# Kernel optimization log

Hardware: AMD Instinct MI355X
Metric: run time of the kernel (lower is better)

Reference implementation:

```python
import jax, jax.numpy as jnp
import numpy as np

B, CIN, COUT, K, H, W_SP = 16, 16, 16, 3, 384, 384


def setup_inputs() -> dict:
    key = jax.random.key(0)
    k1, k2 = jax.random.split(key)
    x = jax.random.normal(k1, (B, CIN, H, W_SP), dtype=jnp.float32)
    W = jax.random.normal(k2, (COUT, CIN, K, K), dtype=jnp.float32) * 0.05
    return {"x": x, "W": W}


def reference(x, W):
    b, cin, h, w = x.shape
    cout, _, kh, kw = W.shape
    # torch.where(x < 0, 0, 1): binary activity mask (x == 0 maps to 1)
    mask = (x >= 0).astype(x.dtype)
    # adaptive_avg_pool2d(mask, kh): h % kh == 0 and w % kw == 0, so bins are
    # exact equal-size means -> reshape + mean.  (b, cin, kh, kw)
    att = mask.reshape(b, cin, kh, h // kh, kw, w // kw).mean(axis=(3, 5))
    att = att.reshape(b, cin, kh * kw)
    att = kh * kw * jax.nn.softmax(att, axis=2) - 1.0
    att = 1.0 + jax.nn.sigmoid(att).reshape(b, cin, kh, kw)
    # per-sample modulated weights: (b, cout, cin, kh, kw); broadcast over cout
    wmod = W[None, :, :, :, :] * att[:, None, :, :, :]

    def conv_one(xi, wi):
        # xi: (cin, h, w), wi: (cout, cin, kh, kw); stride 1, padding 1 (same)
        return jax.lax.conv_general_dilated(
            xi[None], wi, window_strides=(1, 1), padding=[(1, 1), (1, 1)],
            dimension_numbers=("NCHW", "OIHW", "NCHW"))[0]

    # equivalent to the groups=b grouped-conv trick, but without materializing
    # the (1, b*cin, h, w) view
    y = jax.vmap(conv_one)(x, wmod)  # (b, cout, h, w)
    return y
```

## Files before the change

kernel.cpp:

```cpp
#include <hip/hip_runtime.h>
#include <hip/hip_bf16.h>
#include <math.h>

#define BB   16
#define CI   16
#define CO   16
#define HH   384
#define WW   384
#define HW   (HH * WW)

#define PW 386

#define TSW 32
#define TSH 16
#define HSW 34
#define HSH 18
#define NPX (HSW * HSH)

typedef __bf16 bfx8 __attribute__((ext_vector_type(8)));
typedef float  f32x4 __attribute__((ext_vector_type(4)));

__device__ __forceinline__ uint32_t pack_bf16(float a, float b) {
  uint32_t ua = __builtin_bit_cast(uint32_t, a);
  uint32_t ub = __builtin_bit_cast(uint32_t, b);
  ua = (ua + 0x7FFFu + ((ua >> 16) & 1u)) >> 16;
  ub = (ub + 0x7FFFu + ((ub >> 16) & 1u)) >> 16;
  return ua | (ub << 16);
}

__device__ __forceinline__ void gl_lds16(const void* g, void* l) {
  __builtin_amdgcn_global_load_lds(
      (const __attribute__((address_space(1))) uint32_t*)g,
      (__attribute__((address_space(3))) uint32_t*)l, 16, 0, 0);
}


__global__ __launch_bounds__(384, 2) void prep_kernel(
    const float* __restrict__ x, uint4* __restrict__ XP,
    int* __restrict__ pooled) {
  const int b   = blockIdx.y;
  const int blk = blockIdx.x;
  const int tid = threadIdx.x;

  const int r  = tid / 96;
  const int c4 = tid - r * 96;
  const int h  = blk * 4 + r;
  const int w  = c4 * 4;
  const float* px = x + ((size_t)b * CI) * HW + (size_t)h * WW + w;

  f32x4 v[CI];
#pragma unroll
  for (int ci = 0; ci < CI; ++ci)
    v[ci] = *(const f32x4*)(px + (size_t)ci * HW);
  __builtin_amdgcn_sched_barrier(0);

  uint4* dst = XP + (((size_t)b * PW + (h + 1)) * PW + (w + 1)) * 2;
#pragma unroll
  for (int p = 0; p < 4; ++p) {
    uint32_t pk[8];
#pragma unroll
    for (int i = 0; i < 8; ++i)
      pk[i] = pack_bf16(v[2 * i][p], v[2 * i + 1][p]);
    uint4 lo, hi;
    lo.x = pk[0]; lo.y = pk[1]; lo.z = pk[2]; lo.w = pk[3];
    hi.x = pk[4]; hi.y = pk[5]; hi.z = pk[6]; hi.w = pk[7];
    dst[2 * p]     = lo;
    dst[2 * p + 1] = hi;
  }

  int cnt[CI];
#pragma unroll
  for (int ci = 0; ci < CI; ++ci)
    cnt[ci] = (v[ci][0] >= 0.f) + (v[ci][1] >= 0.f) + (v[ci][2] >= 0.f) +
              (v[ci][3] >= 0.f);

#pragma unroll
  for (int ci = 0; ci < CI; ++ci) {
#pragma unroll
    for (int s = 1; s < 32; s <<= 1)
      cnt[ci] += __shfl_xor(cnt[ci], s, 64);
  }

  if ((tid & 31) == 0) {
    const int bin = (h >> 7) * 3 + (w >> 7);
#pragma unroll
    for (int ci = 0; ci < CI; ++ci)
      atomicAdd(&pooled[(b * CI + ci) * 9 + bin], cnt[ci]);
  }
}

__global__ __launch_bounds__(384) void border_kernel(uint4* __restrict__ XP) {
  const int b = blockIdx.x;
  const int tid = threadIdx.x;
  const uint4 z = {0u, 0u, 0u, 0u};
  for (int j = tid; j < 1540; j += 384) {
    int pr, pc;
    if (j < 386)       { pr = 0;            pc = j; }
    else if (j < 772)  { pr = PW - 1;       pc = j - 386; }
    else if (j < 1156) { pr = j - 772 + 1;  pc = 0; }
    else               { pr = j - 1156 + 1; pc = PW - 1; }
    uint4* p = XP + (((size_t)b * PW + pr) * PW + pc) * 2;
    p[0] = z; p[1] = z;
  }
}

__global__ __launch_bounds__(256) void att_finish_int(
    const int* __restrict__ pooled, float* __restrict__ att) {
  const int plane = threadIdx.x;
  float v[9];
#pragma unroll
  for (int k = 0; k < 9; ++k)
    v[k] = (float)pooled[plane * 9 + k] * (1.f / 16384.f);
  float m = v[0];
#pragma unroll
  for (int k = 1; k < 9; ++k) m = fmaxf(m, v[k]);
  float e[9], s = 0.f;
#pragma unroll
  for (int k = 0; k < 9; ++k) { e[k] = expf(v[k] - m); s += e[k]; }
  const float inv = 1.f / s;
#pragma unroll
  for (int k = 0; k < 9; ++k) {
    const float a = 9.f * e[k] * inv - 1.f;
    att[plane * 9 + k] = 1.f + 1.f / (1.f + expf(-a));
  }
}

__global__ __launch_bounds__(256) void conv_fast(
    const char* __restrict__ XPc, const float* __restrict__ Wt,
    const float* __restrict__ att, float* __restrict__ y) {
  const int b   = blockIdx.z;
  const int gx0 = blockIdx.x * TSW;
  const int gy0 = blockIdx.y * TSH;
  const int tid = threadIdx.x;

  __shared__ __align__(16) uint32_t sx[NPX * 8];
  __shared__ __align__(16) uint32_t sw[CO * 80];

  const int lane = tid & 63;
  const int wv   = tid >> 6;

  const char* XPb = XPc + (size_t)b * (PW * PW * 32);
#pragma unroll
  for (int i = wv; i < 20; i += 4) {
    const int chunk = i * 64 + lane;
    const int px  = chunk >> 1;
    const int hf  = chunk & 1;
    const int rr  = px / HSW;
    const int cc  = px - rr * HSW;
    const int swz = (cc >> 2) & 1;
    const char* src =
        XPb + (((size_t)(gy0 + rr) * PW + (gx0 + cc)) << 5) + ((hf ^ swz) << 4);
    if (chunk < 2 * NPX) gl_lds16(src, (char*)sx + i * 1024);
  }

#pragma unroll
  for (int i = 0; i < 5; ++i) {
    const int idx  = tid + 256 * i;
    const int cout = idx / 80;
    const int kp   = idx - cout * 80;
    const int k0 = 2 * kp, k1 = 2 * kp + 1;
    const int p0 = k0 >> 4, ci0 = k0 & 15;
    const int p1 = k1 >> 4, ci1 = k1 & 15;
    float v0 = 0.f, v1 = 0.f;
    if (p0 < 9) v0 = Wt[(cout * CI + ci0) * 9 + p0] * att[(b * CI + ci0) * 9 + p0];
    if (p1 < 9) v1 = Wt[(cout * CI + ci1) * 9 + p1] * att[(b * CI + ci1) * 9 + p1];
    sw[cout * 80 + kp] = pack_bf16(v0, v1);
  }
  __syncthreads();

  const int cpix = lane & 15;
  const int h4   = lane >> 4;
  const int hB   = h4 & 1;
  const int pp   = lane >> 5;

  bfx8 aw[5];
  const char* swb = (const char*)sw;
#pragma unroll
  for (int q = 0; q < 5; ++q)
    aw[q] = *(const bfx8*)(swb + cpix * 320 + q * 64 + h4 * 16);

  int Lq[5];
#pragma unroll
  for (int q = 0; q < 5; ++q) {
    int p = 2 * q + pp;
    if (p > 8) p = 8;
    const int dy = p / 3, dx = p - 3 * dy;
    const int ccl = cpix + dx;
    const int swz = (ccl >> 2) & 1;
    Lq[q] = (dy * HSW + ccl) * 32 + 16 * (hB ^ swz);
  }

  const char* sxb = (const char*)sx;
  float* yb = y + ((size_t)b * CO + h4 * 4) * HW + (size_t)gy0 * WW + gx0 + cpix;

#pragma unroll 2
  for (int ri = 0; ri < 4; ++ri) {
    const int r = wv * 4 + ri;
    const int gbase = (r * HSW) * 32;
    f32x4 a0 = {0.f, 0.f, 0.f, 0.f};
    f32x4 a1 = {0.f, 0.f, 0.f, 0.f};
#pragma unroll
    for (int q = 0; q < 5; ++q) {
      const bfx8 b0 = *(const bfx8*)(sxb + gbase + Lq[q]);
      const bfx8 b1 = *(const bfx8*)(sxb + gbase + 512 + Lq[q]);
      a0 = __builtin_amdgcn_mfma_f32_16x16x32_bf16(aw[q], b0, a0, 0, 0, 0);
      a1 = __builtin_amdgcn_mfma_f32_16x16x32_bf16(aw[q], b1, a1, 0, 0, 0);
    }
    float* yr = yb + (size_t)r * WW;
#pragma unroll
    for (int j = 0; j < 4; ++j) {
      __builtin_nontemporal_store(a0[j], &yr[(size_t)j * HW]);
      __builtin_nontemporal_store(a1[j], &yr[(size_t)j * HW + 16]);
    }
  }
}

__global__ __launch_bounds__(256) void pool_kernel(
    const float* __restrict__ x, float* __restrict__ pooled) {
  const int bx = blockIdx.x;
  const int plane = bx / 9;
  const int bin = bx - plane * 9;
  const int br = (bin / 3) * 128;
  const int bc4 = (bin % 3) * 32;
  const float4* xp = (const float4*)(x + (size_t)plane * HW);
  const int tid = threadIdx.x;
  int cnt = 0;
#pragma unroll
  for (int k = 0; k < 16; ++k) {
    const int idx = tid + k * 256;
    const int r = idx >> 5;
    const int c4 = idx & 31;
    const float4 v = xp[(size_t)(br + r) * (WW / 4) + bc4 + c4];
    cnt += (v.x >= 0.f) + (v.y >= 0.f) + (v.z >= 0.f) + (v.w >= 0.f);
  }
#pragma unroll
  for (int s = 32; s > 0; s >>= 1) cnt += __shfl_down(cnt, s);
  __shared__ int wsum[4];
  const int lane = tid & 63, wid = tid >> 6;
  if (lane == 0) wsum[wid] = cnt;
  __syncthreads();
  if (tid == 0)
    pooled[bx] = (float)(wsum[0] + wsum[1] + wsum[2] + wsum[3]) * (1.f / 16384.f);
}

__global__ __launch_bounds__(256) void att_finish(
    const float* __restrict__ pooled, float* __restrict__ att) {
  const int plane = threadIdx.x;
  float v[9];
#pragma unroll
  for (int k = 0; k < 9; ++k) v[k] = pooled[plane * 9 + k];
  float m = v[0];
#pragma unroll
  for (int k = 1; k < 9; ++k) m = fmaxf(m, v[k]);
  float e[9], s = 0.f;
#pragma unroll
  for (int k = 0; k < 9; ++k) { e[k] = expf(v[k] - m); s += e[k]; }
  const float inv = 1.f / s;
#pragma unroll
  for (int k = 0; k < 9; ++k) {
    const float a = 9.f * e[k] * inv - 1.f;
    att[plane * 9 + k] = 1.f + 1.f / (1.f + expf(-a));
  }
}

__global__ __launch_bounds__(256) void conv_legacy(
    const float* __restrict__ x, const float* __restrict__ Wt,
    const float* __restrict__ att, float* __restrict__ y) {
  const int b   = blockIdx.z;
  const int gx0 = blockIdx.x * TSW;
  const int gy0 = blockIdx.y * TSH;
  const int tid = threadIdx.x;
  __shared__ __align__(16) uint32_t sx[NPX * 8];
  __shared__ __align__(16) uint32_t sw[CO * 80];
  const float* xb = x + (size_t)b * CI * HW;
#pragma unroll
  for (int i = 0; i < 5; ++i) {
    const int idx  = tid + 256 * i;
    const int cout = idx / 80;
    const int kp   = idx - cout * 80;
    const int k0 = 2 * kp, k1 = 2 * kp + 1;
    const int p0 = k0 >> 4, ci0 = k0 & 15;
    const int p1 = k1 >> 4, ci1 = k1 & 15;
    float v0 = 0.f, v1 = 0.f;
    if (p0 < 9) v0 = Wt[(cout * CI + ci0) * 9 + p0] * att[(b * CI + ci0) * 9 + p0];
    if (p1 < 9) v1 = Wt[(cout * CI + ci1) * 9 + p1] * att[(b * CI + ci1) * 9 + p1];
    sw[cout * 80 + kp] = pack_bf16(v0, v1);
  }
#pragma unroll
  for (int it = 0; it < 3; ++it) {
    const int pix = tid + 256 * it;
    if (pix < NPX) {
      const int rr = pix / HSW;
      const int cc = pix - rr * HSW;
      const int gr = gy0 - 1 + rr;
      const int gc = gx0 - 1 + cc;
      uint32_t pk[8];
      if (((unsigned)gr < (unsigned)HH) && ((unsigned)gc < (unsigned)WW)) {
        const float* px = xb + (size_t)gr * WW + gc;
#pragma unroll
        for (int i = 0; i < 8; ++i)
          pk[i] = pack_bf16(px[(size_t)(2 * i) * HW], px[(size_t)(2 * i + 1) * HW]);
      } else {
#pragma unroll
        for (int i = 0; i < 8; ++i) pk[i] = 0u;
      }
      const int s = (cc >> 2) & 1;
      uint32_t* dst = &sx[pix * 8];
      uint4 lo, hi;
      lo.x = pk[0]; lo.y = pk[1]; lo.z = pk[2]; lo.w = pk[3];
      hi.x = pk[4]; hi.y = pk[5]; hi.z = pk[6]; hi.w = pk[7];
      *(uint4*)(dst + 4 * s)       = lo;
      *(uint4*)(dst + 4 * (1 - s)) = hi;
    }
  }
  __syncthreads();
  const int lane = tid & 63;
  const int wv   = tid >> 6;
  const int cpix = lane & 15;
  const int h4   = lane >> 4;
  const int hB   = h4 & 1;
  const int pp   = lane >> 5;
  bfx8 aw[5];
  const char* swb = (const char*)sw;
#pragma unroll
  for (int q = 0; q < 5; ++q)
    aw[q] = *(const bfx8*)(swb + cpix * 320 + q * 64 + h4 * 16);
  int Lq[5];
#pragma unroll
  for (int q = 0; q < 5; ++q) {
    int p = 2 * q + pp;
    if (p > 8) p = 8;
    const int dy = p / 3, dx = p - 3 * dy;
    const int ccl = cpix + dx;
    const int swz = (ccl >> 2) & 1;
    Lq[q] = (dy * HSW + ccl) * 32 + 16 * (hB ^ swz);
  }
  const char* sxb = (const char*)sx;
  float* yb = y + ((size_t)b * CO + h4 * 4) * HW + (size_t)gy0 * WW + gx0 + cpix;
#pragma unroll 2
  for (int ri = 0; ri < 4; ++ri) {
    const int r = wv * 4 + ri;
    const int gbase = (r * HSW) * 32;
    f32x4 a0 = {0.f, 0.f, 0.f, 0.f};
    f32x4 a1 = {0.f, 0.f, 0.f, 0.f};
#pragma unroll
    for (int q = 0; q < 5; ++q) {
      const bfx8 b0 = *(const bfx8*)(sxb + gbase + Lq[q]);
      const bfx8 b1 = *(const bfx8*)(sxb + gbase + 512 + Lq[q]);
      a0 = __builtin_amdgcn_mfma_f32_16x16x32_bf16(aw[q], b0, a0, 0, 0, 0);
      a1 = __builtin_amdgcn_mfma_f32_16x16x32_bf16(aw[q], b1, a1, 0, 0, 0);
    }
    float* yr = yb + (size_t)r * WW;
#pragma unroll
    for (int j = 0; j < 4; ++j) {
      yr[(size_t)j * HW]      = a0[j];
      yr[(size_t)j * HW + 16] = a1[j];
    }
  }
}

extern "C" void kernel_launch(void* const* d_in, const int* in_sizes, int n_in,
                              void* d_out, int out_size, void* d_ws,
                              size_t ws_size, hipStream_t stream) {
  const float* x  = (const float*)d_in[0];
  const float* Wt = (const float*)d_in[1];
  float* y = (float*)d_out;
  char* wsb = (char*)d_ws;

  const size_t need = 65536 + (size_t)BB * PW * PW * 32;
  if (ws_size >= need) {
    int*   pooled = (int*)wsb;
    float* att    = (float*)(wsb + 16384);
    uint4* XP     = (uint4*)(wsb + 65536);
    hipMemsetAsync(pooled, 0, BB * CI * 9 * sizeof(int), stream);
    border_kernel<<<dim3(BB), dim3(384), 0, stream>>>(XP);
    prep_kernel<<<dim3(96, BB), dim3(384), 0, stream>>>(x, XP, pooled);
    att_finish_int<<<dim3(1), dim3(256), 0, stream>>>(pooled, att);
    conv_fast<<<dim3(WW / TSW, HH / TSH, BB), dim3(256), 0, stream>>>(
        (const char*)XP, Wt, att, y);
  } else {
    float* pooled = (float*)wsb;
    float* att    = (float*)wsb + 4096;
    pool_kernel<<<dim3(BB * CI * 9), dim3(256), 0, stream>>>(x, pooled);
    att_finish<<<dim3(1), dim3(256), 0, stream>>>(pooled, att);
    conv_legacy<<<dim3(WW / TSW, HH / TSH, BB), dim3(256), 0, stream>>>(
        x, Wt, att, y);
  }
}
```

Before: 146.5 us.

## Stage prep input rows through LDS with direct global-to-LDS loads

The bf16 packing/prep kernel now loads two full input rows for all 16 channels into shared memory using global_load_lds, then has each thread transpose one pixel per row into channel-interleaved bf16 and write contiguous 32-byte chunks. Before, each thread held 16 float4 registers and wrote four pixels' worth of strided stores. The aim is to coalesce the output stores, reduce register pressure and overlap the loads. In exchange it adds an LDS round trip, a block barrier and twice as many blocks.

```diff
diff --git a/kernel.cpp b/kernel.cpp
--- a/kernel.cpp
+++ b/kernel.cpp
@@ -17,6 +17,8 @@
 #define HSH 18
 #define NPX (HSW * HSH)
 
+#define PSTR 772
+
 typedef __bf16 bfx8 __attribute__((ext_vector_type(8)));
 typedef float  f32x4 __attribute__((ext_vector_type(4)));
 
@@ -35,44 +37,52 @@
 }
 
 
-__global__ __launch_bounds__(384, 2) void prep_kernel(
+__global__ __launch_bounds__(384) void prep_kernel(
     const float* __restrict__ x, uint4* __restrict__ XP,
     int* __restrict__ pooled) {
   const int b   = blockIdx.y;
-  const int blk = blockIdx.x;
-  const int tid = threadIdx.x;
-
-  const int r  = tid / 96;
-  const int c4 = tid - r * 96;
-  const int h  = blk * 4 + r;
-  const int w  = c4 * 4;
-  const float* px = x + ((size_t)b * CI) * HW + (size_t)h * WW + w;
-
-  f32x4 v[CI];
-#pragma unroll
-  for (int ci = 0; ci < CI; ++ci)
-    v[ci] = *(const f32x4*)(px + (size_t)ci * HW);
-  __builtin_amdgcn_sched_barrier(0);
-
-  uint4* dst = XP + (((size_t)b * PW + (h + 1)) * PW + (w + 1)) * 2;
-#pragma unroll
-  for (int p = 0; p < 4; ++p) {
+  const int h0  = blockIdx.x * 2;
+  const int tid = threadIdx.x;
+  const int lane = tid & 63;
+  const int wv   = tid >> 6;
+
+  __shared__ __align__(16) uint32_t sxs[CI * PSTR];
+
+  const float* xb = x + (size_t)b * CI * HW + (size_t)h0 * WW;
+#pragma unroll
+  for (int i = 0; i < 8; ++i) {
+    const int j  = wv * 8 + i;
+    const int pl = j / 3;
+    const int k  = j - pl * 3;
+    const float* src = xb + (size_t)pl * HW + k * 256 + lane * 4;
+    gl_lds16(src, (char*)sxs + pl * (PSTR * 4) + k * 1024);
+  }
+  __syncthreads();
+
+  int cnt[CI];
+#pragma unroll
+  for (int ci = 0; ci < CI; ++ci) cnt[ci] = 0;
+
+#pragma unroll
+  for (int half = 0; half < 2; ++half) {
+    const int p = tid + half * 384;
     uint32_t pk[8];
 #pragma unroll
-    for (int i = 0; i < 8; ++i)
-      pk[i] = pack_bf16(v[2 * i][p], v[2 * i + 1][p]);
+    for (int i = 0; i < 8; ++i) {
+      const float v0 = __builtin_bit_cast(float, sxs[(2 * i) * PSTR + p]);
+      const float v1 = __builtin_bit_cast(float, sxs[(2 * i + 1) * PSTR + p]);
+      cnt[2 * i]     += (v0 >= 0.f);
+      cnt[2 * i + 1] += (v1 >= 0.f);
+      pk[i] = pack_bf16(v0, v1);
+    }
     uint4 lo, hi;
     lo.x = pk[0]; lo.y = pk[1]; lo.z = pk[2]; lo.w = pk[3];
     hi.x = pk[4]; hi.y = pk[5]; hi.z = pk[6]; hi.w = pk[7];
-    dst[2 * p]     = lo;
-    dst[2 * p + 1] = hi;
-  }
-
-  int cnt[CI];
-#pragma unroll
-  for (int ci = 0; ci < CI; ++ci)
-    cnt[ci] = (v[ci][0] >= 0.f) + (v[ci][1] >= 0.f) + (v[ci][2] >= 0.f) +
-              (v[ci][3] >= 0.f);
+    uint4* dst =
+        XP + (((size_t)b * PW + (h0 + half + 1)) * PW + (tid + 1)) * 2;
+    dst[0] = lo;
+    dst[1] = hi;
+  }
 
 #pragma unroll
   for (int ci = 0; ci < CI; ++ci) {
@@ -80,9 +90,8 @@
     for (int s = 1; s < 32; s <<= 1)
       cnt[ci] += __shfl_xor(cnt[ci], s, 64);
   }
-
   if ((tid & 31) == 0) {
-    const int bin = (h >> 7) * 3 + (w >> 7);
+    const int bin = (h0 >> 7) * 3 + (tid >> 7);
 #pragma unroll
     for (int ci = 0; ci < CI; ++ci)
       atomicAdd(&pooled[(b * CI + ci) * 9 + bin], cnt[ci]);
@@ -374,7 +383,7 @@
     uint4* XP     = (uint4*)(wsb + 65536);
     hipMemsetAsync(pooled, 0, BB * CI * 9 * sizeof(int), stream);
     border_kernel<<<dim3(BB), dim3(384), 0, stream>>>(XP);
-    prep_kernel<<<dim3(96, BB), dim3(384), 0, stream>>>(x, XP, pooled);
+    prep_kernel<<<dim3(HH / 2, BB), dim3(384), 0, stream>>>(x, XP, pooled);
     att_finish_int<<<dim3(1), dim3(256), 0, stream>>>(pooled, att);
     conv_fast<<<dim3(WW / TSW, HH / TSH, BB), dim3(256), 0, stream>>>(
         (const char*)XP, Wt, att, y);
```

New measurement: 309.4 us. +111.2%, slower.
